# Performance work log

Measured on AMD Instinct MI355X. Metric: run time of the kernel, lower is better.

The kernel has to match this reference:

```python
import jax, jax.numpy as jnp
import numpy as np

D_MODEL = 512
N_HEADS = 8
HIDDEN = 2048  # mlp_ratio * d_model
B, N = 2, 1024

# 2^dim sign-flip frames for FrameAveraging(dim=2)
_FRAME_OPS = jnp.array([[1., 1.], [1., -1.], [-1., 1.], [-1., -1.]], jnp.float32)


def _ln(x, g, b, eps=1e-5):
    mu = jnp.mean(x, axis=-1, keepdims=True)
    var = jnp.mean((x - mu) ** 2, axis=-1, keepdims=True)
    return (x - mu) * jax.lax.rsqrt(var + eps) * g + b


def setup_inputs() -> dict:
    key = jax.random.key(0)
    ks = jax.random.split(key, 8)
    s = 0.02
    return {
        "token_embs": jax.random.normal(ks[0], (B, N, D_MODEL), jnp.float32),
        "coords": jax.random.normal(ks[1], (B, N, 2), jnp.float32),
        "padding_mask": jnp.zeros((B, N, N), jnp.bool_),
        "ln1_g": jnp.ones((D_MODEL,), jnp.float32),
        "ln1_b": jnp.zeros((D_MODEL,), jnp.float32),
        "w_qkv": jax.random.normal(ks[2], (D_MODEL, 3 * D_MODEL), jnp.float32) * s,
        "b_qkv": jnp.zeros((3 * D_MODEL,), jnp.float32),
        "w_edge": jax.random.normal(ks[3], (3, N_HEADS), jnp.float32) * s,
        "w_out": jax.random.normal(ks[4], (D_MODEL, D_MODEL), jnp.float32) * s,
        "b_out": jnp.zeros((D_MODEL,), jnp.float32),
        "ln2_g": jnp.ones((D_MODEL,), jnp.float32),
        "ln2_b": jnp.zeros((D_MODEL,), jnp.float32),
        "w1": jax.random.normal(ks[5], (D_MODEL, HIDDEN), jnp.float32) * s,
        "b1": jnp.zeros((HIDDEN,), jnp.float32),
        "w2": jax.random.normal(ks[6], (HIDDEN, D_MODEL), jnp.float32) * s,
        "b2": jnp.zeros((D_MODEL,), jnp.float32),
    }


def _block(x, coords, pad_mask, ln1_g, ln1_b, w_qkv, b_qkv, w_edge, w_out, b_out,
           ln2_g, ln2_b, w1, b1, w2, b2):
    Bb, Nn, C = x.shape
    H = w_edge.shape[1]
    d = C // H
    scale = d ** -0.5
    nf = _FRAME_OPS.shape[0]

    # ---- attention QKV ----
    qkv = _ln(x, ln1_g, ln1_b) @ w_qkv + b_qkv
    q, k, v = jnp.split(qkv, 3, axis=-1)
    q = q.reshape(Bb, Nn, H, d).transpose(0, 2, 1, 3) * scale  # (B,H,N,d)
    k = k.reshape(Bb, Nn, H, d).transpose(0, 2, 1, 3)
    v = v.reshape(Bb, Nn, H, d).transpose(0, 2, 1, 3)
    attn = jnp.einsum('bhnd,bhmd->bhnm', q, k)

    # ---- pairwise radial coords + frame averaging ----
    rc = coords[:, :, None, :] - coords[:, None, :, :]           # (B,N,N,2)
    rnorm = jnp.linalg.norm(rc, axis=-1).reshape(Bb * Nn, Nn, 1)
    rc = rc.reshape(Bb * Nn, Nn, 2)                              # (M,N,2)
    valid = (~pad_mask).reshape(Bb * Nn, Nn)
    m = valid.astype(rc.dtype)[..., None]                        # (M,N,1)
    center = jnp.sum(rc * m, axis=1) / jnp.sum(m, axis=1)        # masked mean
    Xc = (rc - center[:, None]) * m                              # (M,N,2)
    Cov = jnp.einsum('mni,mnj->mij', Xc, Xc)                     # (M,2,2)
    _, V = jnp.linalg.eigh(jax.lax.stop_gradient(Cov))           # PCA frame (detached)
    F_ops = _FRAME_OPS[None, :, None, :] * V[:, None]            # (M,nf,2,2) sign-flipped eigvecs
    h = jnp.einsum('moji,mpj->mopi', F_ops, Xc) * m[:, None]     # (M,nf,N,2)

    feat = jnp.concatenate(
        [h, jnp.broadcast_to(rnorm[:, None], (Bb * Nn, nf, Nn, 1))], axis=-1)  # (M,nf,N,3)
    bias = jnp.einsum('monk,kh->monh', feat, w_edge).mean(axis=1)  # (M,N,H)
    bias = bias.reshape(Bb, Nn, Nn, H).transpose(0, 3, 1, 2)       # (B,H,N,N)

    attn = attn + bias
    attn = jnp.where(pad_mask[:, None], jnp.float32(-1e9), attn)
    attn = jax.nn.softmax(attn, axis=-1)
    o = jnp.einsum('bhnm,bhmd->bhnd', attn, v)
    o = o.transpose(0, 2, 1, 3).reshape(Bb, Nn, C) @ w_out + b_out

    x = x + o
    y = _ln(x, ln2_g, ln2_b)
    y = jax.nn.gelu(y @ w1 + b1, approximate=False) @ w2 + b2
    return x + y


def reference(token_embs, coords, padding_mask, ln1_g, ln1_b, w_qkv, b_qkv, w_edge,
              w_out, b_out, ln2_g, ln2_b, w1, b1, w2, b2):
    return _block(token_embs, coords, padding_mask, ln1_g, ln1_b, w_qkv, b_qkv,
                  w_edge, w_out, b_out, ln2_g, ln2_b, w1, b1, w2, b2)
```

## Files before the change

kernel.cpp:

```cpp
#include <hip/hip_runtime.h>
#include <hip/hip_bf16.h>
#include <math.h>

#define NHEADS 8
#define NTOK   1024
#define MTOK   2048

typedef __attribute__((ext_vector_type(8))) short  sh8;
typedef __attribute__((ext_vector_type(8))) __bf16 bf16x8;
typedef __attribute__((ext_vector_type(4))) float  f32x4;
typedef __attribute__((ext_vector_type(4))) unsigned int u32x4;

__device__ __forceinline__ short f2bf(float v) {
    return __builtin_bit_cast(short, __float2bfloat16(v));
}
__device__ __forceinline__ float bf2f(short v) {
    return __builtin_bit_cast(float, ((unsigned)(unsigned short)v) << 16);
}
__device__ __forceinline__ float ex2(float v) {
    return __builtin_amdgcn_exp2f(v);
}
__device__ __forceinline__ f32x4 mfma16(sh8 a, sh8 b, f32x4 c) {
    return __builtin_amdgcn_mfma_f32_16x16x32_bf16(
        __builtin_bit_cast(bf16x8, a), __builtin_bit_cast(bf16x8, b), c, 0, 0, 0);
}
__device__ __forceinline__ void aload16(void* lds, const void* g) {
    __builtin_amdgcn_global_load_lds(
        (const __attribute__((address_space(1))) unsigned int*)g,
        (__attribute__((address_space(3))) unsigned int*)lds, 16, 0, 0);
}

#define LOG2E 1.4426950408889634f

__global__ __launch_bounds__(256) void ln_bf16(const float* __restrict__ x,
    const float* __restrict__ g, const float* __restrict__ bta, short* __restrict__ y)
{
    int row = blockIdx.x, t = threadIdx.x;
    const float* xr = x + (size_t)row * 512;
    float2 v = *reinterpret_cast<const float2*>(&xr[t*2]);
    float s = v.x + v.y, ss = v.x*v.x + v.y*v.y;
    #pragma unroll
    for (int m = 1; m < 64; m <<= 1) { s += __shfl_xor(s, m); ss += __shfl_xor(ss, m); }
    __shared__ float red[8];
    int wid = t >> 6, lane = t & 63;
    if (!lane) { red[wid] = s; red[4+wid] = ss; }
    __syncthreads();
    s = red[0]+red[1]+red[2]+red[3]; ss = red[4]+red[5]+red[6]+red[7];
    float mu = s*(1.f/512), var = ss*(1.f/512) - mu*mu, rs = rsqrtf(var + 1e-5f);
    float2 gg = *reinterpret_cast<const float2*>(&g[t*2]);
    float2 bb = *reinterpret_cast<const float2*>(&bta[t*2]);
    short2 o; o.x = f2bf((v.x-mu)*rs*gg.x + bb.x); o.y = f2bf((v.y-mu)*rs*gg.y + bb.y);
    *reinterpret_cast<short2*>(&y[(size_t)row*512 + t*2]) = o;
}

__global__ __launch_bounds__(256) void wconv2x(
    const float* __restrict__ W0, short* __restrict__ WT0, int K0, int N0, int nb0,
    const float* __restrict__ W1, short* __restrict__ WT1, int K1, int N1)
{
    const float* W; short* WT; int K, N, bid;
    if ((int)blockIdx.x < nb0) { W = W0; WT = WT0; K = K0; N = N0; bid = blockIdx.x; }
    else                       { W = W1; WT = WT1; K = K1; N = N1; bid = blockIdx.x - nb0; }
    int nbx = N >> 5;
    int bn = (bid % nbx) * 32, bk = (bid / nbx) * 32;
    __shared__ float t[32][33];
    int c = threadIdx.x & 31, r8 = threadIdx.x >> 5;
    #pragma unroll
    for (int i = 0; i < 4; ++i) {
        int r = r8 + i*8;
        t[r][c] = W[(size_t)(bk + r)*N + bn + c];
    }
    __syncthreads();
    #pragma unroll
    for (int i = 0; i < 4; ++i) {
        int r = r8 + i*8;
        WT[(size_t)(bn + r)*K + bk + c] = f2bf(t[c][r]);
    }
}

__global__ __launch_bounds__(256) void prep(const float* __restrict__ coords,
    const unsigned char* __restrict__ mask, short* __restrict__ rnP,
    unsigned long long* __restrict__ mbP)
{
    __shared__ float2 kc_s[64];
    __shared__ float2 qc_s[16];
    int bid = blockIdx.x;
    int bqt = bid >> 4, jt = bid & 15;
    int b = bqt >> 6, qt = bqt & 63;
    int t = threadIdx.x, w = t >> 6, lane = t & 63;
    int lr = lane & 15, lg = lane >> 4;

    if (t < 64)            kc_s[t]      = *reinterpret_cast<const float2*>(&coords[(size_t)(b*1024 + jt*64 + t)*2]);
    else if (t < 80)       qc_s[t - 64] = *reinterpret_cast<const float2*>(&coords[(size_t)(b*1024 + qt*16 + (t - 64))*2]);
    __syncthreads();

    float2 qc = qc_s[lr];
    short4 o;
    short* op = &o.x;
    #pragma unroll
    for (int r = 0; r < 4; ++r) {
        float2 kc = kc_s[w*16 + lg*4 + r];
        float dx = qc.x - kc.x, dy = qc.y - kc.y;
        op[r] = f2bf(sqrtf(dx*dx + dy*dy));
    }
    *reinterpret_cast<short4*>(&rnP[(size_t)((bid*4 + w)*256) + lane*4]) = o;

    #pragma unroll
    for (int i = 0; i < 4; ++i) {
        int q = w*4 + i;
        unsigned char v = mask[(size_t)(b*1024 + qt*16 + q)*NTOK + jt*64 + lane];
        unsigned long long bits = __ballot(v != 0);
        if (!lane) mbP[(size_t)bid*16 + q] = bits;
    }
}

template<int EPI, bool OUTBF, bool BIAS_ROW, bool QSC, int NT, bool VTOUT>
__global__ __launch_bounds__(256) void gemm64(
    const short* __restrict__ A, const short* __restrict__ BT,
    const float* __restrict__ bias, const float* __restrict__ res,
    void* __restrict__ Cout, short* __restrict__ vtx,
    int M, int N, int K, int nbx, int ldc)
{
    __shared__ sh8 As8[3][512];
    __shared__ sh8 Bs8[3][512];
    int tid = threadIdx.x;
    int w = tid >> 6, lane = tid & 63, lr = lane & 15, lg = lane >> 4;
    int wr = w >> 1, wc = w & 1;
    int cpx = gridDim.x >> 3;
    int swz = (blockIdx.x & 7)*cpx + (blockIdx.x >> 3);
    int bx = swz % nbx, by = swz / nbx;
    int bm0 = by*64, bn0 = bx*64;

    f32x4 zero = {0.f,0.f,0.f,0.f};
    f32x4 acc[2][2];
    #pragma unroll
    for (int m = 0; m < 2; ++m)
        #pragma unroll
        for (int n = 0; n < 2; ++n) acc[m][n] = zero;

    #define STAGE(buf, k0) { \
        _Pragma("unroll") \
        for (int it = 0; it < 2; ++it) { \
            int s = tid + it*256; \
            int r = s >> 3, g = s & 7; \
            int ksw = (k0) + ((g ^ (r & 7)) << 3); \
            aload16(&As8[buf][s], A  + (size_t)(bm0 + r)*K + ksw); \
            aload16(&Bs8[buf][s], BT + (size_t)(bn0 + r)*K + ksw); \
        } }

    STAGE(0, 0)
    if (NT > 1) STAGE(1, 64)

    #pragma unroll
    for (int t = 0; t < NT; ++t) {
        if (t + 1 < NT) asm volatile("s_waitcnt vmcnt(4)" ::: "memory");
        else            asm volatile("s_waitcnt vmcnt(0)" ::: "memory");
        __builtin_amdgcn_s_barrier();
        __builtin_amdgcn_sched_barrier(0);
        int buf = t % 3;
        sh8 af[2][2], bfv[2][2];
        #pragma unroll
        for (int m = 0; m < 2; ++m) {
            int R = wr*32 + m*16 + lr;
            #pragma unroll
            for (int s = 0; s < 2; ++s) af[m][s] = As8[buf][R*8 + ((s*4+lg) ^ (R & 7))];
        }
        #pragma unroll
        for (int n = 0; n < 2; ++n) {
            int R = wc*32 + n*16 + lr;
            #pragma unroll
            for (int s = 0; s < 2; ++s) bfv[n][s] = Bs8[buf][R*8 + ((s*4+lg) ^ (R & 7))];
        }
        if (t + 2 < NT) STAGE((t+2)%3, (t+2)*64)
        #pragma unroll
        for (int m = 0; m < 2; ++m)
            #pragma unroll
            for (int n = 0; n < 2; ++n)
                #pragma unroll
                for (int s = 0; s < 2; ++s)
                    acc[m][n] = mfma16(af[m][s], bfv[n][s], acc[m][n]);
        asm volatile("s_waitcnt lgkmcnt(0)" ::: "memory");
    }
    #undef STAGE

    if (VTOUT && bn0 >= 1024) {
        __syncthreads();
        short* tb = (short*)&As8[0][0];
        #pragma unroll
        for (int m = 0; m < 2; ++m)
            #pragma unroll
            for (int n = 0; n < 2; ++n)
                #pragma unroll
                for (int r = 0; r < 4; ++r) {
                    int row = wr*32 + m*16 + lg*4 + r;
                    int col = wc*32 + n*16 + lr;
                    float v = acc[m][n][r] + bias[bn0 + col];
                    tb[col*68 + row] = f2bf(v);
                }
        __syncthreads();
        int vd = tid >> 2, t0 = (tid & 3) << 4;
        #pragma unroll
        for (int i = 0; i < 4; ++i) {
            short4 s4 = *reinterpret_cast<short4*>(&tb[vd*68 + t0 + i*4]);
            *reinterpret_cast<short4*>(&vtx[(size_t)(bn0 - 1024 + vd)*2048 + bm0 + t0 + i*4]) = s4;
        }
        return;
    }

    #pragma unroll
    for (int m = 0; m < 2; ++m) {
        #pragma unroll
        for (int n = 0; n < 2; ++n) {
            #pragma unroll
            for (int r = 0; r < 4; ++r) {
                int row = bm0 + wr*32 + m*16 + lg*4 + r;
                int col = bn0 + wc*32 + n*16 + lr;
                float v = acc[m][n][r] + (BIAS_ROW ? bias[row] : bias[col]);
                if (QSC && col < 512) v *= (0.125f * LOG2E);
                if (EPI == 1) v += res[(size_t)row*ldc + col];
                if (EPI == 2) v = 0.5f * v * (1.0f + erff(v * 0.70710678f));
                if (OUTBF) ((short*)Cout)[(size_t)row*ldc + col] = f2bf(v);
                else       ((float*)Cout)[(size_t)row*ldc + col] = v;
            }
        }
    }
}

template<int EPI, bool OUTBF, bool BIAS_ROW, int NT>
__global__ __launch_bounds__(256) void gemm32n(
    const short* __restrict__ A, const short* __restrict__ BT,
    const float* __restrict__ bias, const float* __restrict__ res,
    void* __restrict__ Cout, int M, int N, int K, int nbx)
{
    __shared__ sh8 As8[3][512];
    __shared__ sh8 Bs8[3][256];
    int tid = threadIdx.x;
    int w = tid >> 6, lane = tid & 63, lr = lane & 15, lg = lane >> 4;
    int cpx = gridDim.x >> 3;
    int swz = (blockIdx.x & 7)*cpx + (blockIdx.x >> 3);
    int bx = swz % nbx, by = swz / nbx;
    int bm0 = by*64, bn0 = bx*32;

    f32x4 zero = {0.f,0.f,0.f,0.f};
    f32x4 acc[2];
    acc[0] = zero; acc[1] = zero;

    #define STAGE32(buf, k0) { \
        _Pragma("unroll") \
        for (int it = 0; it < 2; ++it) { \
            int s = tid + it*256; \
            int r = s >> 3, g = s & 7; \
            int ksw = (k0) + ((g ^ (r & 7)) << 3); \
            aload16(&As8[buf][s], A + (size_t)(bm0 + r)*K + ksw); \
        } \
        { int r = tid >> 3, g = tid & 7; \
          int ksw = (k0) + ((g ^ (r & 7)) << 3); \
          aload16(&Bs8[buf][tid], BT + (size_t)(bn0 + r)*K + ksw); } }

    STAGE32(0, 0)
    if (NT > 1) STAGE32(1, 64)

    #pragma unroll
    for (int t = 0; t < NT; ++t) {
        if (t + 1 < NT) asm volatile("s_waitcnt vmcnt(3)" ::: "memory");
        else            asm volatile("s_waitcnt vmcnt(0)" ::: "memory");
        __builtin_amdgcn_s_barrier();
        __builtin_amdgcn_sched_barrier(0);
        int buf = t % 3;
        sh8 af[2], bfv[2][2];
        int Ra = w*16 + lr;
        #pragma unroll
        for (int s = 0; s < 2; ++s) af[s] = As8[buf][Ra*8 + ((s*4+lg) ^ (Ra & 7))];
        #pragma unroll
        for (int n = 0; n < 2; ++n) {
            int R = n*16 + lr;
            #pragma unroll
            for (int s = 0; s < 2; ++s) bfv[n][s] = Bs8[buf][R*8 + ((s*4+lg) ^ (R & 7))];
        }
        if (t + 2 < NT) STAGE32((t+2)%3, (t+2)*64)
        #pragma unroll
        for (int n = 0; n < 2; ++n)
            #pragma unroll
            for (int s = 0; s < 2; ++s)
                acc[n] = mfma16(af[s], bfv[n][s], acc[n]);
        asm volatile("s_waitcnt lgkmcnt(0)" ::: "memory");
    }
    #undef STAGE32

    #pragma unroll
    for (int n = 0; n < 2; ++n) {
        #pragma unroll
        for (int r = 0; r < 4; ++r) {
            int row = bm0 + w*16 + lg*4 + r;
            int col = bn0 + n*16 + lr;
            float v = acc[n][r] + (BIAS_ROW ? bias[row] : bias[col]);
            if (EPI == 1) v += res[(size_t)row*N + col];
            if (EPI == 2) v = 0.5f * v * (1.0f + erff(v * 0.70710678f));
            if (OUTBF) ((short*)Cout)[(size_t)row*N + col] = f2bf(v);
            else       ((float*)Cout)[(size_t)row*N + col] = v;
        }
    }
}

__global__ __launch_bounds__(512) void attn_reg(
    const short* __restrict__ qk, const short* __restrict__ vt,
    const short* __restrict__ rnP, const unsigned long long* __restrict__ mbP,
    const float* __restrict__ w_edge, short* __restrict__ OpA,
    short* __restrict__ OpB, float* __restrict__ ml)
{
    __shared__ sh8 Ks8[2][512];
    __shared__ sh8 Vs8[2][512];

    int cpx = gridDim.x >> 3;
    int swz = (blockIdx.x & 7)*cpx + (blockIdx.x >> 3);
    int w = threadIdx.x >> 6, lane = threadIdx.x & 63;
    int lr = lane & 15, lg = lane >> 4;
    int qb = swz & 7;
    int h  = (swz >> 3) & 7;
    int b  = (swz >> 6) & 1;
    int ks = swz >> 7;

    const int q0 = qb*128 + w*16;
    const int qrow0 = b*NTOK + q0;
    const int jt0 = ks*4;
    const int bqt = b*64 + qb*8 + w;

    sh8 qf[2];
    #pragma unroll
    for (int s = 0; s < 2; ++s)
        qf[s] = *reinterpret_cast<const sh8*>(qk + (size_t)(qrow0 + lr)*1024 + h*64 + s*32 + lg*8);

    float we2l = w_edge[2*NHEADS + h] * LOG2E;

    float m_i = -1e30f, l_lane = 0.f;
    f32x4 zero = {0.f,0.f,0.f,0.f};
    f32x4 accO[4];
    #pragma unroll
    for (int n = 0; n < 4; ++n) accO[n] = zero;

    const short* kbase = qk + 512 + h*64;
    const short* vbase = vt + (size_t)h*64*2048 + b*NTOK;
    int sr = threadIdx.x >> 3, sg = threadIdx.x & 7;
    int sx = (sg ^ (sr & 7)) << 3;

    #define ASTAGE(bf, jt) { \
        aload16(&Ks8[bf][threadIdx.x], kbase + (size_t)(b*NTOK + (jt)*64 + sr)*1024 + sx); \
        aload16(&Vs8[bf][threadIdx.x], vbase + (size_t)sr*2048 + (jt)*64 + sx); \
    }

    short4 rn_reg[2][4];
    unsigned long long mr_reg[2];
    #define RMLOAD(bf, jt) { \
        _Pragma("unroll") \
        for (int n = 0; n < 4; ++n) \
            rn_reg[bf][n] = *reinterpret_cast<const short4*>( \
                &rnP[(size_t)(((bqt*16 + (jt))*4 + n)*256) + lane*4]); \
        mr_reg[bf] = mbP[(size_t)(bqt*16 + (jt))*16 + lr]; \
    }

    ASTAGE(0, jt0)
    RMLOAD(0, jt0)

    #pragma unroll
    for (int t = 0; t < 4; ++t) {
        asm volatile("s_waitcnt vmcnt(5)" ::: "memory");
        __builtin_amdgcn_s_barrier();
        __builtin_amdgcn_sched_barrier(0);
        int buf = t & 1;

        if (t + 1 < 4) {
            ASTAGE(buf ^ 1, jt0 + t + 1)
            RMLOAD(buf ^ 1, jt0 + t + 1)
        }

        f32x4 Sv[4];
        #pragma unroll
        for (int n = 0; n < 4; ++n) {
            int kcol = n*16 + lr;
            sh8 k0v = Ks8[buf][kcol*8 + (lg       ^ (kcol & 7))];
            sh8 k1v = Ks8[buf][kcol*8 + ((4 + lg) ^ (kcol & 7))];
            Sv[n] = mfma16(k1v, qf[1], mfma16(k0v, qf[0], zero));
        }

        #pragma unroll
        for (int n = 0; n < 4; ++n) {
            short4 rn4 = rn_reg[buf][n];
            Sv[n][0] = fmaf(bf2f(rn4.x), we2l, Sv[n][0]);
            Sv[n][1] = fmaf(bf2f(rn4.y), we2l, Sv[n][1]);
            Sv[n][2] = fmaf(bf2f(rn4.z), we2l, Sv[n][2]);
            Sv[n][3] = fmaf(bf2f(rn4.w), we2l, Sv[n][3]);
        }

        float mx = Sv[0][0];
        #pragma unroll
        for (int n = 0; n < 4; ++n)
            #pragma unroll
            for (int r = 0; r < 4; ++r) mx = fmaxf(mx, Sv[n][r]);
        mx = fmaxf(mx, __shfl_xor(mx, 16));
        mx = fmaxf(mx, __shfl_xor(mx, 32));

        if (!__all(mx <= m_i + 8.0f)) {
            float mnew = fmaxf(m_i, mx);
            float f = ex2(m_i - mnew);
            m_i = mnew;
            l_lane *= f;
            float fb[4];
            #pragma unroll
            for (int r = 0; r < 4; ++r) fb[r] = __shfl(f, lg*4 + r);
            #pragma unroll
            for (int n = 0; n < 4; ++n)
                #pragma unroll
                for (int r = 0; r < 4; ++r) accO[n][r] *= fb[r];
        }

        unsigned long long mr = mr_reg[buf];
        float ps = 0.f;
        unsigned pk[8];
        #pragma unroll
        for (int n = 0; n < 4; ++n) {
            float p_[4];
            #pragma unroll
            for (int r = 0; r < 4; ++r) {
                float p = ex2(Sv[n][r] - m_i);
                p = ((mr >> (n*16 + lg*4 + r)) & 1ull) ? 0.f : p;
                ps += p;
                p_[r] = p;
            }
            asm("v_cvt_pk_bf16_f32 %0, %1, %2" : "=v"(pk[2*n])   : "v"(p_[0]), "v"(p_[1]));
            asm("v_cvt_pk_bf16_f32 %0, %1, %2" : "=v"(pk[2*n+1]) : "v"(p_[2]), "v"(p_[3]));
        }
        l_lane += ps;

        int src0 = lr + ((lg & 1) << 5);
        int src1 = src0 + 16;
        sh8 pa[2];
        #pragma unroll
        for (int s = 0; s < 2; ++s) {
            int ns = 2*s + (lg >> 1);
            u32x4 dv;
            dv.x = (unsigned)__shfl((int)pk[2*ns],   src0);
            dv.y = (unsigned)__shfl((int)pk[2*ns+1], src0);
            dv.z = (unsigned)__shfl((int)pk[2*ns],   src1);
            dv.w = (unsigned)__shfl((int)pk[2*ns+1], src1);
            pa[s] = __builtin_bit_cast(sh8, dv);
        }

        #pragma unroll
        for (int n = 0; n < 4; ++n) {
            int dcol = n*16 + lr;
            sh8 v0 = Vs8[buf][dcol*8 + (lg       ^ (dcol & 7))];
            sh8 v1 = Vs8[buf][dcol*8 + ((4 + lg) ^ (dcol & 7))];
            accO[n] = mfma16(pa[1], v1, mfma16(pa[0], v0, accO[n]));
        }

        asm volatile("s_waitcnt lgkmcnt(0)" ::: "memory");
    }
    #undef ASTAGE
    #undef RMLOAD

    l_lane += __shfl_xor(l_lane, 16);
    l_lane += __shfl_xor(l_lane, 32);

    short* Op = (ks < 2) ? OpA : OpB;
    #pragma unroll
    for (int r = 0; r < 4; ++r) {
        size_t row = (size_t)((ks & 1)*MTOK + qrow0 + lg*4 + r);
        #pragma unroll
        for (int n = 0; n < 4; ++n)
            Op[row*512 + h*64 + n*16 + lr] = f2bf(accO[n][r]);
    }
    if (lg == 0) {
        size_t mrow = (size_t)(ks*MTOK + qrow0 + lr);
        ml[(mrow*NHEADS + h)*2 + 0] = m_i;
        ml[(mrow*NHEADS + h)*2 + 1] = l_lane;
    }
}

__global__ __launch_bounds__(256) void attn_combine4(const short* __restrict__ OpA,
    const short* __restrict__ OpB, const float* __restrict__ ml,
    short* __restrict__ ob)
{
    int idx = blockIdx.x*256 + threadIdx.x;
    int tok = idx >> 7, dd = (idx & 127) * 4;
    int h = dd >> 6;
    float m[4], l[4];
    #pragma unroll
    for (int s = 0; s < 4; ++s) {
        m[s] = ml[(((size_t)s*MTOK + tok)*NHEADS + h)*2 + 0];
        l[s] = ml[(((size_t)s*MTOK + tok)*NHEADS + h)*2 + 1];
    }
    float mm = fmaxf(fmaxf(m[0], m[1]), fmaxf(m[2], m[3]));
    float wsum = 0.f, a0 = 0.f, a1 = 0.f, a2 = 0.f, a3 = 0.f;
    #pragma unroll
    for (int s = 0; s < 4; ++s) {
        float wv = ex2(m[s] - mm);
        wsum += wv * l[s];
        const short* Op = (s < 2) ? OpA : OpB;
        short4 p = *reinterpret_cast<const short4*>(&Op[((size_t)((s&1)*MTOK) + tok)*512 + dd]);
        a0 += bf2f(p.x)*wv; a1 += bf2f(p.y)*wv;
        a2 += bf2f(p.z)*wv; a3 += bf2f(p.w)*wv;
    }
    float inv = 1.f / wsum;
    short4 o;
    o.x = f2bf(a0*inv); o.y = f2bf(a1*inv);
    o.z = f2bf(a2*inv); o.w = f2bf(a3*inv);
    *reinterpret_cast<short4*>(&ob[(size_t)tok*512 + dd]) = o;
}

extern "C" void kernel_launch(void* const* d_in, const int* in_sizes, int n_in,
                              void* d_out, int out_size, void* d_ws, size_t ws_size,
                              hipStream_t stream)
{
    const float* x      = (const float*)d_in[0];
    const float* coords = (const float*)d_in[1];
    const unsigned char* mask = (const unsigned char*)d_in[2];
    const float* ln1_g = (const float*)d_in[3];
    const float* ln1_b = (const float*)d_in[4];
    const float* w_qkv = (const float*)d_in[5];
    const float* b_qkv = (const float*)d_in[6];
    const float* w_edge= (const float*)d_in[7];
    const float* w_out = (const float*)d_in[8];
    const float* b_out = (const float*)d_in[9];
    const float* ln2_g = (const float*)d_in[10];
    const float* ln2_b = (const float*)d_in[11];
    const float* w1    = (const float*)d_in[12];
    const float* b1    = (const float*)d_in[13];
    const float* w2    = (const float*)d_in[14];
    const float* b2    = (const float*)d_in[15];
    float* out = (float*)d_out;

    char* W = (char*)d_ws;
    const size_t MB = 1024*1024;
    float* x1    = (float*)(W);
    short* qk    = (short*)(W + 4*MB);
    short* vtb   = (short*)(W + 8*MB);
    short* woutT = (short*)(W + 10*MB);
    short* xln   = (short*)(W + 10*MB + 512*1024);
    short* wqkvT = (short*)(W + 12*MB + 512*1024);
    short* OpB   = (short*)(W + 10*MB + 512*1024);
    short* OpA   = (short*)(W + 14*MB + 512*1024);
    short* rnP   = (short*)(W + 18*MB + 512*1024);
    float* mlp   = (float*)(W + 22*MB + 512*1024);
    unsigned long long* mbP = (unsigned long long*)(W + 23*MB);
    short* ob    = (short*)(W + 6*MB);
    short* y     = xln;
    short* w1T   = (short*)(W + 4*MB);
    short* w2T   = (short*)(W + 8*MB);
    short* hid   = (short*)(W + 14*MB + 512*1024);

    prep<<<dim3(2048,1,1), 256, 0, stream>>>(coords, mask, rnP, mbP);
    wconv2x<<<dim3(1024,1,1), 256, 0, stream>>>(w_qkv, wqkvT, 512, 1536, 768,
                                                w_out, woutT, 512, 512);
    ln_bf16<<<MTOK, 256, 0, stream>>>(x, ln1_g, ln1_b, xln);
    gemm64<0,true,false,true,8,true><<<dim3(768,1,1), 256, 0, stream>>>(
        xln, wqkvT, b_qkv, nullptr, qk, vtb, MTOK, 1536, 512, 24, 1024);
    attn_reg<<<dim3(512,1,1), 512, 0, stream>>>(qk, vtb, rnP, mbP, w_edge, OpA, OpB, mlp);
    attn_combine4<<<dim3(1024,1,1), 256, 0, stream>>>(OpA, OpB, mlp, ob);
    gemm32n<1,false,false,8><<<dim3(512,1,1), 256, 0, stream>>>(
        ob, woutT, b_out, x, x1, MTOK, 512, 512, 16);
    wconv2x<<<dim3(2048,1,1), 256, 0, stream>>>(w1, w1T, 512, 2048, 1024,
                                                w2, w2T, 2048, 512);
    ln_bf16<<<MTOK, 256, 0, stream>>>(x1, ln2_g, ln2_b, y);
    gemm64<2,true,false,false,8,false><<<dim3(1024,1,1), 256, 0, stream>>>(
        y, w1T, b1, nullptr, hid, nullptr, MTOK, 2048, 512, 32, 2048);
    gemm32n<1,false,false,32><<<dim3(512,1,1), 256, 0, stream>>>(
        hid, w2T, b2, x1, out, MTOK, 512, 2048, 16);
}
```

Baseline: 85.41 us.

## Merge prep with weight conversion and preload all attention tiles upfront

The prep kernel and the first weight-transpose kernel are fused into one launch, with blocks past 2048 doing the weight conversion, so one kernel launch goes away. In attn_reg the double-buffered K/V pipeline is replaced by loading all four K/V tiles and all bias and mask registers up front, followed by a single wait and barrier. This removes the per-iteration barriers and waits, but doubles LDS use and raises register pressure, which may lower occupancy and lose overlap between loads and compute.

```diff
diff --git a/kernel.cpp b/kernel.cpp
--- a/kernel.cpp
+++ b/kernel.cpp
@@ -77,10 +77,34 @@
     }
 }
 
-__global__ __launch_bounds__(256) void prep(const float* __restrict__ coords,
-    const unsigned char* __restrict__ mask, short* __restrict__ rnP,
-    unsigned long long* __restrict__ mbP)
-{
+__global__ __launch_bounds__(256) void prep_wconv(
+    const float* __restrict__ coords, const unsigned char* __restrict__ mask,
+    short* __restrict__ rnP, unsigned long long* __restrict__ mbP,
+    const float* __restrict__ W0, short* __restrict__ WT0,
+    const float* __restrict__ W1, short* __restrict__ WT1)
+{
+    if ((int)blockIdx.x >= 2048) {
+        int bid = blockIdx.x - 2048;
+        const float* W; short* WT; int N;
+        if (bid < 768) { W = W0; WT = WT0; N = 1536; }
+        else           { W = W1; WT = WT1; N = 512; bid -= 768; }
+        int nbx = N >> 5;
+        int bn = (bid % nbx) * 32, bk = (bid / nbx) * 32;
+        __shared__ float t[32][33];
+        int c = threadIdx.x & 31, r8 = threadIdx.x >> 5;
+        #pragma unroll
+        for (int i = 0; i < 4; ++i) {
+            int r = r8 + i*8;
+            t[r][c] = W[(size_t)(bk + r)*N + bn + c];
+        }
+        __syncthreads();
+        #pragma unroll
+        for (int i = 0; i < 4; ++i) {
+            int r = r8 + i*8;
+            WT[(size_t)(bn + r)*512 + bk + c] = f2bf(t[c][r]);
+        }
+        return;
+    }
     __shared__ float2 kc_s[64];
     __shared__ float2 qc_s[16];
     int bid = blockIdx.x;
@@ -307,8 +331,8 @@
     const float* __restrict__ w_edge, short* __restrict__ OpA,
     short* __restrict__ OpB, float* __restrict__ ml)
 {
-    __shared__ sh8 Ks8[2][512];
-    __shared__ sh8 Vs8[2][512];
+    __shared__ sh8 Ks8[4][512];
+    __shared__ sh8 Vs8[4][512];
 
     int cpx = gridDim.x >> 3;
     int swz = (blockIdx.x & 7)*cpx + (blockIdx.x >> 3);
@@ -342,48 +366,39 @@
     int sr = threadIdx.x >> 3, sg = threadIdx.x & 7;
     int sx = (sg ^ (sr & 7)) << 3;
 
-    #define ASTAGE(bf, jt) { \
-        aload16(&Ks8[bf][threadIdx.x], kbase + (size_t)(b*NTOK + (jt)*64 + sr)*1024 + sx); \
-        aload16(&Vs8[bf][threadIdx.x], vbase + (size_t)sr*2048 + (jt)*64 + sx); \
-    }
-
-    short4 rn_reg[2][4];
-    unsigned long long mr_reg[2];
-    #define RMLOAD(bf, jt) { \
-        _Pragma("unroll") \
-        for (int n = 0; n < 4; ++n) \
-            rn_reg[bf][n] = *reinterpret_cast<const short4*>( \
-                &rnP[(size_t)(((bqt*16 + (jt))*4 + n)*256) + lane*4]); \
-        mr_reg[bf] = mbP[(size_t)(bqt*16 + (jt))*16 + lr]; \
-    }
-
-    ASTAGE(0, jt0)
-    RMLOAD(0, jt0)
-
     #pragma unroll
     for (int t = 0; t < 4; ++t) {
-        asm volatile("s_waitcnt vmcnt(5)" ::: "memory");
-        __builtin_amdgcn_s_barrier();
-        __builtin_amdgcn_sched_barrier(0);
-        int buf = t & 1;
-
-        if (t + 1 < 4) {
-            ASTAGE(buf ^ 1, jt0 + t + 1)
-            RMLOAD(buf ^ 1, jt0 + t + 1)
-        }
-
+        aload16(&Ks8[t][threadIdx.x], kbase + (size_t)(b*NTOK + (jt0 + t)*64 + sr)*1024 + sx);
+        aload16(&Vs8[t][threadIdx.x], vbase + (size_t)sr*2048 + (jt0 + t)*64 + sx);
+    }
+    short4 rn_reg[4][4];
+    unsigned long long mr_reg[4];
+    #pragma unroll
+    for (int t = 0; t < 4; ++t) {
+        #pragma unroll
+        for (int n = 0; n < 4; ++n)
+            rn_reg[t][n] = *reinterpret_cast<const short4*>(
+                &rnP[(size_t)(((bqt*16 + jt0 + t)*4 + n)*256) + lane*4]);
+        mr_reg[t] = mbP[(size_t)(bqt*16 + jt0 + t)*16 + lr];
+    }
+
+    asm volatile("s_waitcnt vmcnt(0)" ::: "memory");
+    __builtin_amdgcn_s_barrier();
+
+    #pragma unroll
+    for (int t = 0; t < 4; ++t) {
         f32x4 Sv[4];
         #pragma unroll
         for (int n = 0; n < 4; ++n) {
             int kcol = n*16 + lr;
-            sh8 k0v = Ks8[buf][kcol*8 + (lg       ^ (kcol & 7))];
-            sh8 k1v = Ks8[buf][kcol*8 + ((4 + lg) ^ (kcol & 7))];
+            sh8 k0v = Ks8[t][kcol*8 + (lg       ^ (kcol & 7))];
+            sh8 k1v = Ks8[t][kcol*8 + ((4 + lg) ^ (kcol & 7))];
             Sv[n] = mfma16(k1v, qf[1], mfma16(k0v, qf[0], zero));
         }
 
         #pragma unroll
         for (int n = 0; n < 4; ++n) {
-            short4 rn4 = rn_reg[buf][n];
+            short4 rn4 = rn_reg[t][n];
             Sv[n][0] = fmaf(bf2f(rn4.x), we2l, Sv[n][0]);
             Sv[n][1] = fmaf(bf2f(rn4.y), we2l, Sv[n][1]);
             Sv[n][2] = fmaf(bf2f(rn4.z), we2l, Sv[n][2]);
@@ -412,7 +427,7 @@
                 for (int r = 0; r < 4; ++r) accO[n][r] *= fb[r];
         }
 
-        unsigned long long mr = mr_reg[buf];
+        unsigned long long mr = mr_reg[t];
         float ps = 0.f;
         unsigned pk[8];
         #pragma unroll
@@ -447,15 +462,11 @@
         #pragma unroll
         for (int n = 0; n < 4; ++n) {
             int dcol = n*16 + lr;
-            sh8 v0 = Vs8[buf][dcol*8 + (lg       ^ (dcol & 7))];
-            sh8 v1 = Vs8[buf][dcol*8 + ((4 + lg) ^ (dcol & 7))];
+            sh8 v0 = Vs8[t][dcol*8 + (lg       ^ (dcol & 7))];
+            sh8 v1 = Vs8[t][dcol*8 + ((4 + lg) ^ (dcol & 7))];
             accO[n] = mfma16(pa[1], v1, mfma16(pa[0], v0, accO[n]));
         }
-
-        asm volatile("s_waitcnt lgkmcnt(0)" ::: "memory");
-    }
-    #undef ASTAGE
-    #undef RMLOAD
+    }
 
     l_lane += __shfl_xor(l_lane, 16);
     l_lane += __shfl_xor(l_lane, 32);
@@ -547,9 +558,8 @@
     short* w2T   = (short*)(W + 8*MB);
     short* hid   = (short*)(W + 14*MB + 512*1024);
 
-    prep<<<dim3(2048,1,1), 256, 0, stream>>>(coords, mask, rnP, mbP);
-    wconv2x<<<dim3(1024,1,1), 256, 0, stream>>>(w_qkv, wqkvT, 512, 1536, 768,
-                                                w_out, woutT, 512, 512);
+    prep_wconv<<<dim3(3072,1,1), 256, 0, stream>>>(coords, mask, rnP, mbP,
+                                                   w_qkv, wqkvT, w_out, woutT);
     ln_bf16<<<MTOK, 256, 0, stream>>>(x, ln1_g, ln1_b, xln);
     gemm64<0,true,false,true,8,true><<<dim3(768,1,1), 256, 0, stream>>>(
         xln, wqkvT, b_qkv, nullptr, qk, vtb, MTOK, 1536, 512, 24, 1024);
```

Result: faster. 83.54 us (-2.2%).
